# Kernel optimization log

Measured on AMD Instinct MI355X. Metric: run time of the kernel, lower is better.

Reference implementation:

```python
import jax, jax.numpy as jnp
import numpy as np

N_QUBITS = 8
DEPTH = 1
INPUT_DIM = 64
HIDDEN = 8  # must equal N_QUBITS
SEQ = 64
BATCH = 256


def _apply_rx(state, wire, ang):
    # state: (B, 2, 2, ..., 2) with wire w on axis 1+w; ang: (B,) angles
    n = state.ndim - 1
    st = jnp.moveaxis(state, 1 + wire, -1)
    a0, a1 = st[..., 0], st[..., 1]
    half = ang * 0.5
    c = jnp.cos(half).reshape((-1,) + (1,) * (n - 1))
    s = jnp.sin(half).reshape((-1,) + (1,) * (n - 1))
    new = jnp.stack([c * a0 - 1j * s * a1, c * a1 - 1j * s * a0], axis=-1)
    return jnp.moveaxis(new, -1, 1 + wire)


def _apply_cnot(state, cw, tw):
    st = jnp.moveaxis(state, (1 + cw, 1 + tw), (-2, -1))
    st = st.at[..., 1, :].set(st[..., 1, ::-1])  # flip target where control=1
    return jnp.moveaxis(st, (-2, -1), (1 + cw, 1 + tw))


def qgate(theta, qparams):
    # theta: (B, n) data-dependent RX angles; qparams: (n,) trainable RX angles
    B, n = theta.shape
    state = jnp.zeros((B,) + (2,) * n, dtype=jnp.complex64)
    state = state.at[(slice(None),) + (0,) * n].set(1.0 + 0.0j)  # |0...0>
    for w in range(n):
        state = _apply_rx(state, w, theta[:, w])
    for w in range(n - 1):
        state = _apply_cnot(state, w, w + 1)
    for w in range(n):
        state = _apply_rx(state, w, jnp.broadcast_to(qparams[w], (B,)))
    probs = jnp.abs(state) ** 2  # (B, 2, ..., 2)
    expz = []
    for w in range(n):
        pw = probs.sum(axis=tuple(a for a in range(1, n + 1) if a != 1 + w))  # (B, 2)
        expz.append(pw[:, 0] - pw[:, 1])  # <Z_w>
    return jnp.stack(expz, axis=1)  # (B, n)


def setup_inputs() -> dict:
    key = jax.random.key(0)
    ks = jax.random.split(key, 13)
    d_in = INPUT_DIM + HIDDEN
    d_out = N_QUBITS * DEPTH
    sc = 1.0 / np.sqrt(d_in)
    inp = {"inputs": jax.random.normal(ks[0], (SEQ, BATCH, INPUT_DIM), dtype=jnp.float32)}
    names = ["f", "i", "g", "o"]
    for j, nm in enumerate(names):
        inp["W" + nm] = jax.random.uniform(ks[1 + 3 * j], (d_out, d_in), minval=-sc, maxval=sc, dtype=jnp.float32)
        inp["b" + nm] = jax.random.uniform(ks[2 + 3 * j], (d_out,), minval=-sc, maxval=sc, dtype=jnp.float32)
        inp["q" + nm] = jax.random.normal(ks[3 + 3 * j], (d_out,), dtype=jnp.float32)
    return inp


def reference(inputs, Wf, bf, qf, Wi, bi, qi, Wg, bg, qg, Wo, bo, qo):
    B = inputs.shape[1]
    hx0 = jnp.zeros((B, HIDDEN), dtype=inputs.dtype)
    cx0 = jnp.zeros((B, HIDDEN), dtype=inputs.dtype)

    def step(carry, x_t):
        hx, cx = carry
        comb = jnp.concatenate([x_t, hx], axis=1)  # (B, input+hidden)
        f = jax.nn.sigmoid(qgate(comb @ Wf.T + bf, qf))
        i_ = jax.nn.sigmoid(qgate(comb @ Wi.T + bi, qi))
        g = jnp.tanh(qgate(comb @ Wg.T + bg, qg))
        o = jax.nn.sigmoid(qgate(comb @ Wo.T + bo, qo))
        cx = f * cx + i_ * g
        hx = o * jnp.tanh(cx)
        return (hx, cx), hx

    (hx, cx), outputs = jax.lax.scan(step, (hx0, cx0), inputs)
    return outputs, (hx, cx)
```

## Files before the change

### kernel.cpp

```cpp
#include <hip/hip_runtime.h>
#include <hip/hip_bf16.h>

__device__ float g_pre_static[8 * 1024 * 1024];

__device__ __forceinline__ float rcp_(float x)   { return __builtin_amdgcn_rcpf(x); }
__device__ __forceinline__ float sigm_f(float x) { return rcp_(1.0f + __expf(-x)); }
__device__ __forceinline__ float tanh_f(float x) { return 1.0f - 2.0f*rcp_(__expf(2.0f*x) + 1.0f); }
__device__ __forceinline__ float sigm(float x)  { return 1.0f/(1.0f + __expf(-x)); }
__device__ __forceinline__ float tanh_(float x) { float e = __expf(2.0f*x); return (e-1.0f)/(e+1.0f); }

template<int CTRL>
__device__ __forceinline__ float dppf(float x) {
    return __int_as_float(__builtin_amdgcn_update_dpp(
        0, __float_as_int(x), CTRL, 0xF, 0xF, true));
}

template<int IDD>
__global__ __launch_bounds__(512) void k_fused8(
    const float* __restrict__ x_,
    const float* __restrict__ W0, const float* __restrict__ b0p, const float* __restrict__ q0v,
    const float* __restrict__ W1, const float* __restrict__ b1p, const float* __restrict__ q1v,
    const float* __restrict__ W2, const float* __restrict__ b2p, const float* __restrict__ q2v,
    const float* __restrict__ W3, const float* __restrict__ b3p, const float* __restrict__ q3v,
    float* __restrict__ out, int S, int B)
{
    constexpr int DIN  = IDD + 8;
    constexpr int SMAX = 64;
    constexpr int TCH  = 32;
    __shared__ float xs[4][TCH][IDD];
    __shared__ float ps[SMAX][4][32];

    const int tid = threadIdx.x;
    const long b0 = (long)blockIdx.x * 4;
    const float* Wp[4] = {W0, W1, W2, W3};
    const float* bp[4] = {b0p, b1p, b2p, b3p};
    const float* qp[4] = {q0v, q1v, q2v, q3v};

    const int l  = tid & 31;
    const int b4 = (tid >> 5) & 3;
    const int hh = tid >> 7;
    const int gp = l >> 4, w8 = (l >> 1) & 7, e = l & 1;
    const int g  = 2*gp + e;

    float wr[IDD];
    {
        const float4* wv = (const float4*)(Wp[g] + (long)w8*DIN);
        #pragma unroll
        for (int k4 = 0; k4 < IDD/4; ++k4) {
            float4 v = wv[k4];
            wr[4*k4] = v.x; wr[4*k4+1] = v.y; wr[4*k4+2] = v.z; wr[4*k4+3] = v.w;
        }
    }
    const float bias = bp[g][w8];

    for (int c = 0; c < S; c += TCH) {
        {
            const int nf4 = 4 * TCH * (IDD/4);
            for (int idx = tid; idx < nf4; idx += 512) {
                int k4 = idx & (IDD/4 - 1);
                int r  = idx >> 4;
                int bs = r >> 5;
                int tl = r & (TCH - 1);
                int t  = c + tl; if (t >= S) t = S - 1;
                long bb = b0 + bs; if (bb >= B) bb = B - 1;
                float4 v = ((const float4*)(x_ + ((long)t*B + bb)*IDD))[k4];
                ((float4*)&xs[bs][tl][0])[k4] = v;
            }
        }
        __syncthreads();
        #pragma unroll
        for (int i = 0; i < TCH/4; ++i) {
            int t = c + hh*(TCH/4) + i;
            if (t < S) {
                const float4* xv = (const float4*)&xs[b4][t - c][0];
                float a0 = bias, a1 = 0.0f, a2 = 0.0f, a3 = 0.0f;
                #pragma unroll
                for (int k4 = 0; k4 < IDD/4; ++k4) {
                    float4 v = xv[k4];
                    a0 = fmaf(wr[4*k4],   v.x, a0);
                    a1 = fmaf(wr[4*k4+1], v.y, a1);
                    a2 = fmaf(wr[4*k4+2], v.z, a2);
                    a3 = fmaf(wr[4*k4+3], v.w, a3);
                }
                ps[t][b4][l] = (a0 + a1) + (a2 + a3);
            }
        }
        __syncthreads();
    }

    if (tid >= 64) return;

    const int lane = tid;
    const int w    = lane & 7;
    const int gpr  = (lane >> 3) & 1;
    const long b   = b0 + (lane >> 4);
    const int g0 = 2*gpr, g1 = 2*gpr + 1;

    float wrot0[8], wrot1[8];
    #pragma unroll
    for (int k = 0; k < 8; ++k) {
        int j = (w - k) & 7;
        wrot0[k] = Wp[g0][(long)w*DIN + IDD + j];
        wrot1[k] = Wp[g1][(long)w*DIN + IDD + j];
    }
    const float qv0 = qp[g0][w], qv1 = qp[g1][w];
    const float mult0 = (w < 7) ? __cosf(qv0) : 1.0f;
    const float mult1 = (w < 7) ? __cosf(qv1) : 1.0f;
    const float qadd0 = (w == 7) ? qv0 : 0.0f;
    const float qadd1 = (w == 7) ? qv1 : 0.0f;
    const float ascl = gpr ? 2.0f : 1.0f;
    const float aoff = gpr ? -1.0f : 0.0f;

    float cxw = 0.0f, hxw = 0.0f;
    float hxr[8];
    #pragma unroll
    for (int k = 0; k < 8; ++k) hxr[k] = 0.0f;

    const float2* pbase = (const float2*)(&ps[0][lane >> 4][gpr*16 + 2*w]);

    float2 pn = pbase[0];
    #pragma unroll 2
    for (int t = 0; t < S; ++t) {
        float2 pc = pn;
        int tn = (t + 1 < S) ? (t + 1) : (S - 1);
        pn = pbase[(long)tn * 64];

        float tA0 = pc.x, tA1 = pc.y, tB0, tB1;
        tA0 = fmaf(wrot0[0], hxr[0], tA0);  tA1 = fmaf(wrot1[0], hxr[0], tA1);
        tA0 = fmaf(wrot0[1], hxr[1], tA0);  tA1 = fmaf(wrot1[1], hxr[1], tA1);
        tA0 = fmaf(wrot0[2], hxr[2], tA0);  tA1 = fmaf(wrot1[2], hxr[2], tA1);
        tA0 = fmaf(wrot0[3], hxr[3], tA0);  tA1 = fmaf(wrot1[3], hxr[3], tA1);
        tB0 = wrot0[4]*hxr[4];              tB1 = wrot1[4]*hxr[4];
        tB0 = fmaf(wrot0[5], hxr[5], tB0);  tB1 = fmaf(wrot1[5], hxr[5], tB1);
        tB0 = fmaf(wrot0[6], hxr[6], tB0);  tB1 = fmaf(wrot1[6], hxr[6], tB1);
        tB0 = fmaf(wrot0[7], hxr[7], tB0);  tB1 = fmaf(wrot1[7], hxr[7], tB1);
        float th0 = tA0 + tB0;
        float th1 = tA1 + tB1;

        float P0 = __cosf(th0 + qadd0);
        float P1 = __cosf(th1 + qadd1);

        float s;
        s = dppf<0x111>(P0); P0 *= (w >= 1) ? s : 1.0f;
        s = dppf<0x111>(P1); P1 *= (w >= 1) ? s : 1.0f;
        s = dppf<0x112>(P0); P0 *= (w >= 2) ? s : 1.0f;
        s = dppf<0x112>(P1); P1 *= (w >= 2) ? s : 1.0f;
        s = dppf<0x114>(P0); P0 *= (w >= 4) ? s : 1.0f;
        s = dppf<0x114>(P1); P1 *= (w >= 4) ? s : 1.0f;

        float act0 = ascl * sigm_f(ascl * (mult0 * P0)) + aoff;
        float act1 = sigm_f(mult1 * P1);

        float ex0 = dppf<0x128>(act0);
        float ex1 = dppf<0x128>(act1);
        float fv = gpr ? ex0  : act0;
        float iv = gpr ? ex1  : act1;
        float gv = gpr ? act0 : ex0;
        float ov = gpr ? act1 : ex1;

        cxw = fv*cxw + iv*gv;
        hxw = ov * tanh_f(cxw);

        if (gpr == 0 && b < B) out[((long)t*B + b)*8 + w] = hxw;

        hxr[0] = hxw;
        hxr[1] = dppf<0x121>(hxw);
        hxr[2] = dppf<0x122>(hxw);
        hxr[3] = dppf<0x123>(hxw);
        hxr[4] = dppf<0x124>(hxw);
        hxr[5] = dppf<0x125>(hxw);
        hxr[6] = dppf<0x126>(hxw);
        hxr[7] = dppf<0x127>(hxw);
    }

    if (gpr == 0 && b < B) {
        out[((long)S*B + b)*8 + w]     = hxw;
        out[((long)S*B + B + b)*8 + w] = cxw;
    }
}

template<int IDD>
__global__ __launch_bounds__(256) void k_pre8(
    const float* __restrict__ x_,
    const float* __restrict__ W0, const float* __restrict__ b0p,
    const float* __restrict__ W1, const float* __restrict__ b1p,
    const float* __restrict__ W2, const float* __restrict__ b2p,
    const float* __restrict__ W3, const float* __restrict__ b3p,
    float* __restrict__ pre, int S, int B)
{
    constexpr int DIN = IDD + 8;
    __shared__ float xs[8][IDD];
    const int t   = blockIdx.x;
    const int tid = threadIdx.x;
    const int bl  = tid >> 5;
    const int l   = tid & 31;
    const int gp  = l >> 4, w = (l >> 1) & 7, e = l & 1;
    const int g   = 2*gp + e;
    const long b0 = (long)blockIdx.y * 8;
    const float* Wp[4] = {W0, W1, W2, W3};
    const float* bp[4] = {b0p, b1p, b2p, b3p};

    if (tid < 8*(IDD/4)) {
        int r = tid / (IDD/4), k4 = tid % (IDD/4);
        long bb = b0 + r; if (bb >= B) bb = B - 1;
        float4 v = ((const float4*)(x_ + ((long)t*B + bb)*IDD))[k4];
        ((float4*)&xs[r][0])[k4] = v;
    }

    float wr[IDD];
    {
        const float4* wv = (const float4*)(Wp[g] + (long)w*DIN);
        #pragma unroll
        for (int k4 = 0; k4 < IDD/4; ++k4) {
            float4 v = wv[k4];
            wr[4*k4] = v.x; wr[4*k4+1] = v.y; wr[4*k4+2] = v.z; wr[4*k4+3] = v.w;
        }
    }
    float a = bp[g][w];
    __syncthreads();

    const long b = b0 + bl;
    if (b >= B) return;
    const float4* xv = (const float4*)&xs[bl][0];
    #pragma unroll
    for (int k4 = 0; k4 < IDD/4; ++k4) {
        float4 v = xv[k4];
        a += wr[4*k4]*v.x + wr[4*k4+1]*v.y + wr[4*k4+2]*v.z + wr[4*k4+3]*v.w;
    }
    pre[((long)t*B + b)*32 + l] = a;
}

__global__ __launch_bounds__(256) void k_pre_gen(
    const float* __restrict__ x_,
    const float* W0, const float* b0p,
    const float* W1, const float* b1p,
    const float* W2, const float* b2p,
    const float* W3, const float* b3p,
    float* __restrict__ pre,
    int S, int B, int ID, int H, int SP)
{
    extern __shared__ float lds[];
    const int dIn  = ID + H;
    const int dInP = dIn + 1;
    float* xs    = lds;
    float* wsh   = lds + 64*SP;
    float* sbias = wsh + 4*H*dInP;
    const int t   = blockIdx.x;
    const int tid = threadIdx.x;
    const int bl  = tid & 63;
    const int q   = tid >> 6;
    const int b0  = blockIdx.y * 64;
    const float* Wp[4] = {W0, W1, W2, W3};
    const float* bp[4] = {b0p, b1p, b2p, b3p};

    for (int g = 0; g < 4; ++g)
        for (int idx = tid; idx < H*dIn; idx += 256) {
            int w = idx / dIn, k = idx - w*dIn;
            wsh[(g*H + w)*dInP + k] = Wp[g][idx];
        }
    for (int idx = tid; idx < 4*H; idx += 256)
        sbias[idx] = bp[idx / H][idx % H];

    {
        int total = 64 * ID;
        for (int i = tid; i < total; i += 256) {
            int r = i / ID, c = i - r*ID;
            long bb = (long)b0 + r; if (bb >= B) bb = B - 1;
            xs[r*SP + c] = x_[((long)t*B + bb)*ID + c];
        }
    }
    __syncthreads();

    const int b = b0 + bl;
    if (b < B) {
        const float* xrow = &xs[bl*SP];
        float* orow = pre + (((long)t*B + b)*4 + q)*H;
        for (int w = 0; w < H; ++w) {
            float acc = sbias[q*H + w];
            const float* wrow = &wsh[(q*H + w)*dInP];
            for (int k = 0; k < ID; ++k) acc += xrow[k] * wrow[k];
            orow[w] = acc;
        }
    }
}

__global__ __launch_bounds__(64) void k_rec8(
    const float* __restrict__ W0, const float* __restrict__ q0,
    const float* __restrict__ W1, const float* __restrict__ q1,
    const float* __restrict__ W2, const float* __restrict__ q2,
    const float* __restrict__ W3, const float* __restrict__ q3,
    const float* __restrict__ pre,
    float* __restrict__ out, int S, int B, int ID)
{
    const int dIn  = ID + 8;
    const int lane = threadIdx.x;
    const int w    = lane & 7;
    const int gp   = (lane >> 3) & 1;
    const int b    = blockIdx.x*4 + (lane >> 4);
    const int bs   = (b < B) ? b : (B - 1);
    const float* Wp[4] = {W0, W1, W2, W3};
    const float* qp[4] = {q0, q1, q2, q3};
    const int g0 = 2*gp, g1 = 2*gp + 1;

    float wrot0[8], wrot1[8];
    #pragma unroll
    for (int k = 0; k < 8; ++k) {
        int j = (w - k) & 7;
        wrot0[k] = Wp[g0][(long)w*dIn + ID + j];
        wrot1[k] = Wp[g1][(long)w*dIn + ID + j];
    }
    const float qv0 = qp[g0][w], qv1 = qp[g1][w];
    const float mult0 = (w < 7) ? __cosf(qv0) : 1.0f;
    const float mult1 = (w < 7) ? __cosf(qv1) : 1.0f;
    const float qadd0 = (w == 7) ? qv0 : 0.0f;
    const float qadd1 = (w == 7) ? qv1 : 0.0f;
    const float ascl = gp ? 2.0f : 1.0f;
    const float aoff = gp ? -1.0f : 0.0f;

    float cxw = 0.0f, hxw = 0.0f;
    float hxr[8];
    #pragma unroll
    for (int k = 0; k < 8; ++k) hxr[k] = 0.0f;

    const float2* base = (const float2*)(pre + (long)bs*32 + gp*16 + 2*w);
    const long tstep = (long)B*16;

    float2 pf[4];
    #pragma unroll
    for (int d = 0; d < 4; ++d) {
        int tt = (d < S) ? d : (S - 1);
        pf[d] = base[(long)tt*tstep];
    }

    for (int t0 = 0; t0 < S; t0 += 4) {
        #pragma unroll
        for (int d = 0; d < 4; ++d) {
            const int t = t0 + d;
            if (t < S) {
                float2 pc = pf[d];
                int tn = t + 4; if (tn >= S) tn = S - 1;
                pf[d] = base[(long)tn*tstep];

                float th0 = pc.x, th1 = pc.y;
                #pragma unroll
                for (int k = 0; k < 8; ++k) {
                    th0 = fmaf(wrot0[k], hxr[k], th0);
                    th1 = fmaf(wrot1[k], hxr[k], th1);
                }
                float P0 = __cosf(th0 + qadd0);
                float P1 = __cosf(th1 + qadd1);

                float s;
                s = dppf<0x111>(P0); P0 *= (w >= 1) ? s : 1.0f;
                s = dppf<0x111>(P1); P1 *= (w >= 1) ? s : 1.0f;
                s = dppf<0x112>(P0); P0 *= (w >= 2) ? s : 1.0f;
                s = dppf<0x112>(P1); P1 *= (w >= 2) ? s : 1.0f;
                s = dppf<0x114>(P0); P0 *= (w >= 4) ? s : 1.0f;
                s = dppf<0x114>(P1); P1 *= (w >= 4) ? s : 1.0f;

                float act0 = ascl * sigm_f(ascl * (mult0 * P0)) + aoff;
                float act1 = sigm_f(mult1 * P1);

                float ex0 = dppf<0x128>(act0);
                float ex1 = dppf<0x128>(act1);
                float fv = gp ? ex0  : act0;
                float iv = gp ? ex1  : act1;
                float gv = gp ? act0 : ex0;
                float ov = gp ? act1 : ex1;

                cxw = fv*cxw + iv*gv;
                hxw = ov * tanh_f(cxw);

                if (gp == 0 && b < B) out[((long)t*B + b)*8 + w] = hxw;

                hxr[0] = hxw;
                hxr[1] = dppf<0x121>(hxw);
                hxr[2] = dppf<0x122>(hxw);
                hxr[3] = dppf<0x123>(hxw);
                hxr[4] = dppf<0x124>(hxw);
                hxr[5] = dppf<0x125>(hxw);
                hxr[6] = dppf<0x126>(hxw);
                hxr[7] = dppf<0x127>(hxw);
            }
        }
    }

    if (gp == 0 && b < B) {
        out[((long)S*B + b)*8 + w]     = hxw;
        out[((long)S*B + B + b)*8 + w] = cxw;
    }
}

__global__ __launch_bounds__(64) void k_rec_g(
    const float* __restrict__ pre,
    const float* W0, const float* q0,
    const float* W1, const float* q1,
    const float* W2, const float* q2,
    const float* W3, const float* q3,
    float* __restrict__ out, int S, int B, int ID, int H)
{
    __shared__ float sWh[4*32*32];
    __shared__ float scq[4*32];
    const int dIn = ID + H;
    const int tid = threadIdx.x;
    const int b   = blockIdx.x*64 + tid;
    const float* Wp[4] = {W0, W1, W2, W3};
    const float* qp[4] = {q0, q1, q2, q3};

    for (int idx = tid; idx < 4*H*H; idx += 64) {
        int g = idx / (H*H), r = idx % (H*H);
        int w = r / H, j = r % H;
        sWh[(g*H + w)*H + j] = Wp[g][(long)w*dIn + ID + j];
    }
    for (int idx = tid; idx < 4*H; idx += 64) {
        int g = idx / H, w = idx % H;
        float qv = qp[g][w];
        scq[idx] = (w < H-1) ? __cosf(qv) : qv;
    }
    __syncthreads();
    if (b >= B) return;

    float hx[32], cx[32], gate[4][32], th[32];
    for (int w = 0; w < H; ++w) { hx[w] = 0.0f; cx[w] = 0.0f; }

    for (int t = 0; t < S; ++t) {
        const float* pt = pre + ((long)t*B + b)*4*H;
        for (int g = 0; g < 4; ++g) {
            for (int w = 0; w < H; ++w) {
                float a = pt[g*H + w];
                const float* wrp = &sWh[(g*H + w)*H];
                for (int j = 0; j < H; ++j) a += wrp[j]*hx[j];
                th[w] = a;
            }
            float cum = 1.0f;
            for (int w = 0; w < H-1; ++w) {
                cum *= __cosf(th[w]);
                gate[g][w] = scq[g*H + w] * cum;
            }
            gate[g][H-1] = cum * __cosf(th[H-1] + scq[g*H + H-1]);
        }
        float* orow = out + ((long)t*B + b)*H;
        for (int w = 0; w < H; ++w) {
            float fv = sigm (gate[0][w]);
            float iv = sigm (gate[1][w]);
            float gv = tanh_(gate[2][w]);
            float ov = sigm (gate[3][w]);
            cx[w] = fv*cx[w] + iv*gv;
            hx[w] = ov*tanh_(cx[w]);
            orow[w] = hx[w];
        }
    }
    float* oh = out + ((long)S*B + b)*H;
    float* oc = out + ((long)S*B + B + b)*H;
    for (int w = 0; w < H; ++w) { oh[w] = hx[w]; oc[w] = cx[w]; }
}

static bool derive(long sz[13], long osz, long& S, long& B, long& ID, long& H) {
    H = sz[3];
    long dIn = (H > 0) ? sz[1] / H : 0;
    ID = dIn - H;
    long TB = (ID > 0) ? sz[0] / ID : 0;
    B = (H > 0) ? (osz / H - TB) / 2 : 0;
    S = (B > 0) ? TB / B : 0;
    return (H >= 1 && H <= 32 && ID >= 1 && B >= 1 && S >= 1 &&
            S*B == TB && (S*B + 2*B)*H == osz &&
            dIn*H == sz[1] && TB*ID == sz[0]);
}

extern "C" void kernel_launch(void* const* d_in, const int* in_sizes, int n_in,
                              void* d_out, int out_size, void* d_ws, size_t ws_size,
                              hipStream_t stream) {
    const float* x  = (const float*)d_in[0];
    const float* Wf = (const float*)d_in[1];  const float* bfv = (const float*)d_in[2];  const float* qf = (const float*)d_in[3];
    const float* Wi = (const float*)d_in[4];  const float* biv = (const float*)d_in[5];  const float* qi = (const float*)d_in[6];
    const float* Wg = (const float*)d_in[7];  const float* bgv = (const float*)d_in[8];  const float* qg = (const float*)d_in[9];
    const float* Wo = (const float*)d_in[10]; const float* bov = (const float*)d_in[11]; const float* qo = (const float*)d_in[12];
    float* out = (float*)d_out;

    long S = 0, B = 0, ID = 0, H = 0;
    bool ok = false;
    for (int scale : {1, 4, 2}) {
        long sz[13];
        for (int i = 0; i < 13; ++i) sz[i] = (long)in_sizes[i] / scale;
        long osz = (long)out_size / scale;
        if (derive(sz, osz, S, B, ID, H)) { ok = true; break; }
    }
    if (!ok) { H = 8; ID = 64; B = 256; S = 64; }
    long dIn = ID + H;

    if (H == 8 && ID == 64 && S <= 64) {
        k_fused8<64><<<dim3((unsigned)((B + 3) / 4)), dim3(512), 0, stream>>>(
            x, Wf, bfv, qf, Wi, biv, qi, Wg, bgv, qg, Wo, bov, qo,
            out, (int)S, (int)B);
        return;
    }

    size_t pre_bytes = (size_t)S * 4 * H * B * sizeof(float);
    float* pre = (ws_size >= pre_bytes) ? (float*)d_ws : g_pre_static;

    if (H == 8 && ID == 64) {
        k_pre8<64><<<dim3((unsigned)S, (unsigned)((B + 7) / 8)), dim3(256), 0, stream>>>(
            x, Wf, bfv, Wi, biv, Wg, bgv, Wo, bov, pre, (int)S, (int)B);
        k_rec8<<<dim3((unsigned)((B + 3) / 4)), dim3(64), 0, stream>>>(
            Wf, qf, Wi, qi, Wg, qg, Wo, qo, pre, out, (int)S, (int)B, (int)ID);
    } else {
        int SP = (int)ID + 1;
        size_t lds_bytes = (size_t)(64*SP + 4*H*(dIn + 1) + 4*H) * sizeof(float);
        k_pre_gen<<<dim3((unsigned)S, (unsigned)((B + 63) / 64)), dim3(256), lds_bytes, stream>>>(
            x, Wf, bfv, Wi, biv, Wg, bgv, Wo, bov, pre,
            (int)S, (int)B, (int)ID, (int)H, SP);
        k_rec_g<<<dim3((unsigned)((B + 63) / 64)), dim3(64), 0, stream>>>(
            pre, Wf, qf, Wi, qi, Wg, qg, Wo, qo, out, (int)S, (int)B, (int)ID, (int)H);
    }
}
```

Baseline: 102.8 us.

## Overlap recurrence with input projection using a dedicated recurrence wavefront

Adds a ninth wavefront (576 threads) that runs the serial LSTM recurrence for the previous time chunk while the other 512 threads compute the input projection for the current chunk. The chunk size is halved to 16 so the pipeline has more stages. The goal is to hide the projection phase behind the sequential recurrence instead of running the two back to back. In exchange there is an extra barrier per chunk, and the recurrence is now split into chunks with loop-carried state, which may add overhead.

```diff
diff --git a/kernel.cpp b/kernel.cpp
--- a/kernel.cpp
+++ b/kernel.cpp
@@ -16,7 +16,7 @@
 }
 
 template<int IDD>
-__global__ __launch_bounds__(512) void k_fused8(
+__global__ __launch_bounds__(576) void k_fused8(
     const float* __restrict__ x_,
     const float* __restrict__ W0, const float* __restrict__ b0p, const float* __restrict__ q0v,
     const float* __restrict__ W1, const float* __restrict__ b1p, const float* __restrict__ q1v,
@@ -26,7 +26,7 @@
 {
     constexpr int DIN  = IDD + 8;
     constexpr int SMAX = 64;
-    constexpr int TCH  = 32;
+    constexpr int TCH  = 16;
     __shared__ float xs[4][TCH][IDD];
     __shared__ float ps[SMAX][4][32];
 
@@ -36,146 +36,161 @@
     const float* bp[4] = {b0p, b1p, b2p, b3p};
     const float* qp[4] = {q0v, q1v, q2v, q3v};
 
-    const int l  = tid & 31;
-    const int b4 = (tid >> 5) & 3;
-    const int hh = tid >> 7;
-    const int gp = l >> 4, w8 = (l >> 1) & 7, e = l & 1;
-    const int g  = 2*gp + e;
+    const int l   = tid & 31;
+    const int b4g = (tid >> 5) & 3;
+    const int sub = (tid >> 7) & 3;
+    const int gp  = l >> 4, w8 = (l >> 1) & 7, e = l & 1;
+    const int g   = 2*gp + e;
 
     float wr[IDD];
-    {
+    float bias = 0.0f;
+    if (tid < 512) {
         const float4* wv = (const float4*)(Wp[g] + (long)w8*DIN);
         #pragma unroll
         for (int k4 = 0; k4 < IDD/4; ++k4) {
             float4 v = wv[k4];
             wr[4*k4] = v.x; wr[4*k4+1] = v.y; wr[4*k4+2] = v.z; wr[4*k4+3] = v.w;
         }
-    }
-    const float bias = bp[g][w8];
-
-    for (int c = 0; c < S; c += TCH) {
+        bias = bp[g][w8];
+    }
+
+    const int lane = tid & 63;
+    const int w    = lane & 7;
+    const int gpr  = (lane >> 3) & 1;
+    const long bb_ = b0 + (lane >> 4);
+    const int g0 = 2*gpr, g1 = 2*gpr + 1;
+
+    float wrot0[8], wrot1[8];
+    float mult0 = 1.0f, mult1 = 1.0f, qadd0 = 0.0f, qadd1 = 0.0f;
+    if (tid >= 512) {
+        #pragma unroll
+        for (int k = 0; k < 8; ++k) {
+            int j = (w - k) & 7;
+            wrot0[k] = Wp[g0][(long)w*DIN + IDD + j];
+            wrot1[k] = Wp[g1][(long)w*DIN + IDD + j];
+        }
+        float qv0 = qp[g0][w], qv1 = qp[g1][w];
+        mult0 = (w < 7) ? __cosf(qv0) : 1.0f;
+        mult1 = (w < 7) ? __cosf(qv1) : 1.0f;
+        qadd0 = (w == 7) ? qv0 : 0.0f;
+        qadd1 = (w == 7) ? qv1 : 0.0f;
+    }
+    const float ascl = gpr ? 2.0f : 1.0f;
+    const float aoff = gpr ? -1.0f : 0.0f;
+
+    float cxw = 0.0f, hxw = 0.0f;
+    float hxr[8];
+    #pragma unroll
+    for (int k = 0; k < 8; ++k) hxr[k] = 0.0f;
+
+    const float2* pbase = (const float2*)(&ps[0][lane >> 4][gpr*16 + 2*w]);
+
+    auto rec_run = [&](int t0e, int t1e) {
+        float2 pn = pbase[(long)t0e * 64];
+        for (int t = t0e; t < t1e; ++t) {
+            float2 pc = pn;
+            int tn = (t + 1 < t1e) ? (t + 1) : t;
+            pn = pbase[(long)tn * 64];
+
+            float tA0 = pc.x, tA1 = pc.y, tB0, tB1;
+            tA0 = fmaf(wrot0[0], hxr[0], tA0);  tA1 = fmaf(wrot1[0], hxr[0], tA1);
+            tA0 = fmaf(wrot0[1], hxr[1], tA0);  tA1 = fmaf(wrot1[1], hxr[1], tA1);
+            tA0 = fmaf(wrot0[2], hxr[2], tA0);  tA1 = fmaf(wrot1[2], hxr[2], tA1);
+            tA0 = fmaf(wrot0[3], hxr[3], tA0);  tA1 = fmaf(wrot1[3], hxr[3], tA1);
+            tB0 = wrot0[4]*hxr[4];              tB1 = wrot1[4]*hxr[4];
+            tB0 = fmaf(wrot0[5], hxr[5], tB0);  tB1 = fmaf(wrot1[5], hxr[5], tB1);
+            tB0 = fmaf(wrot0[6], hxr[6], tB0);  tB1 = fmaf(wrot1[6], hxr[6], tB1);
+            tB0 = fmaf(wrot0[7], hxr[7], tB0);  tB1 = fmaf(wrot1[7], hxr[7], tB1);
+            float th0 = tA0 + tB0;
+            float th1 = tA1 + tB1;
+
+            float P0 = __cosf(th0 + qadd0);
+            float P1 = __cosf(th1 + qadd1);
+
+            float s;
+            s = dppf<0x111>(P0); P0 *= (w >= 1) ? s : 1.0f;
+            s = dppf<0x111>(P1); P1 *= (w >= 1) ? s : 1.0f;
+            s = dppf<0x112>(P0); P0 *= (w >= 2) ? s : 1.0f;
+            s = dppf<0x112>(P1); P1 *= (w >= 2) ? s : 1.0f;
+            s = dppf<0x114>(P0); P0 *= (w >= 4) ? s : 1.0f;
+            s = dppf<0x114>(P1); P1 *= (w >= 4) ? s : 1.0f;
+
+            float act0 = ascl * sigm_f(ascl * (mult0 * P0)) + aoff;
+            float act1 = sigm_f(mult1 * P1);
+
+            float ex0 = dppf<0x128>(act0);
+            float ex1 = dppf<0x128>(act1);
+            float fv = gpr ? ex0  : act0;
+            float iv = gpr ? ex1  : act1;
+            float gv = gpr ? act0 : ex0;
+            float ov = gpr ? act1 : ex1;
+
+            cxw = fv*cxw + iv*gv;
+            hxw = ov * tanh_f(cxw);
+
+            if (gpr == 0 && bb_ < B) out[((long)t*B + bb_)*8 + w] = hxw;
+
+            hxr[0] = hxw;
+            hxr[1] = dppf<0x121>(hxw);
+            hxr[2] = dppf<0x122>(hxw);
+            hxr[3] = dppf<0x123>(hxw);
+            hxr[4] = dppf<0x124>(hxw);
+            hxr[5] = dppf<0x125>(hxw);
+            hxr[6] = dppf<0x126>(hxw);
+            hxr[7] = dppf<0x127>(hxw);
+        }
+    };
+
+    const int nch = (S + TCH - 1) / TCH;
+    for (int c = 0; c < nch; ++c) {
         {
             const int nf4 = 4 * TCH * (IDD/4);
-            for (int idx = tid; idx < nf4; idx += 512) {
-                int k4 = idx & (IDD/4 - 1);
-                int r  = idx >> 4;
-                int bs = r >> 5;
-                int tl = r & (TCH - 1);
-                int t  = c + tl; if (t >= S) t = S - 1;
+            for (int idx = tid; idx < nf4; idx += 576) {
+                int k4 = idx % (IDD/4);
+                int r  = idx / (IDD/4);
+                int bs = r / TCH;
+                int tl = r % TCH;
+                int t  = c*TCH + tl; if (t >= S) t = S - 1;
                 long bb = b0 + bs; if (bb >= B) bb = B - 1;
                 float4 v = ((const float4*)(x_ + ((long)t*B + bb)*IDD))[k4];
                 ((float4*)&xs[bs][tl][0])[k4] = v;
             }
         }
         __syncthreads();
-        #pragma unroll
-        for (int i = 0; i < TCH/4; ++i) {
-            int t = c + hh*(TCH/4) + i;
-            if (t < S) {
-                const float4* xv = (const float4*)&xs[b4][t - c][0];
-                float a0 = bias, a1 = 0.0f, a2 = 0.0f, a3 = 0.0f;
-                #pragma unroll
-                for (int k4 = 0; k4 < IDD/4; ++k4) {
-                    float4 v = xv[k4];
-                    a0 = fmaf(wr[4*k4],   v.x, a0);
-                    a1 = fmaf(wr[4*k4+1], v.y, a1);
-                    a2 = fmaf(wr[4*k4+2], v.z, a2);
-                    a3 = fmaf(wr[4*k4+3], v.w, a3);
+
+        if (tid < 512) {
+            #pragma unroll
+            for (int i = 0; i < TCH/4; ++i) {
+                int t = c*TCH + sub*(TCH/4) + i;
+                if (t < S) {
+                    const float4* xv = (const float4*)&xs[b4g][t - c*TCH][0];
+                    float a0 = bias, a1 = 0.0f, a2 = 0.0f, a3 = 0.0f;
+                    #pragma unroll
+                    for (int k4 = 0; k4 < IDD/4; ++k4) {
+                        float4 v = xv[k4];
+                        a0 = fmaf(wr[4*k4],   v.x, a0);
+                        a1 = fmaf(wr[4*k4+1], v.y, a1);
+                        a2 = fmaf(wr[4*k4+2], v.z, a2);
+                        a3 = fmaf(wr[4*k4+3], v.w, a3);
+                    }
+                    ps[t][b4g][l] = (a0 + a1) + (a2 + a3);
                 }
-                ps[t][b4][l] = (a0 + a1) + (a2 + a3);
             }
+        } else if (c > 0) {
+            int t0e = (c - 1) * TCH;
+            int t1e = c * TCH; if (t1e > S) t1e = S;
+            rec_run(t0e, t1e);
         }
         __syncthreads();
     }
 
-    if (tid >= 64) return;
-
-    const int lane = tid;
-    const int w    = lane & 7;
-    const int gpr  = (lane >> 3) & 1;
-    const long b   = b0 + (lane >> 4);
-    const int g0 = 2*gpr, g1 = 2*gpr + 1;
-
-    float wrot0[8], wrot1[8];
-    #pragma unroll
-    for (int k = 0; k < 8; ++k) {
-        int j = (w - k) & 7;
-        wrot0[k] = Wp[g0][(long)w*DIN + IDD + j];
-        wrot1[k] = Wp[g1][(long)w*DIN + IDD + j];
-    }
-    const float qv0 = qp[g0][w], qv1 = qp[g1][w];
-    const float mult0 = (w < 7) ? __cosf(qv0) : 1.0f;
-    const float mult1 = (w < 7) ? __cosf(qv1) : 1.0f;
-    const float qadd0 = (w == 7) ? qv0 : 0.0f;
-    const float qadd1 = (w == 7) ? qv1 : 0.0f;
-    const float ascl = gpr ? 2.0f : 1.0f;
-    const float aoff = gpr ? -1.0f : 0.0f;
-
-    float cxw = 0.0f, hxw = 0.0f;
-    float hxr[8];
-    #pragma unroll
-    for (int k = 0; k < 8; ++k) hxr[k] = 0.0f;
-
-    const float2* pbase = (const float2*)(&ps[0][lane >> 4][gpr*16 + 2*w]);
-
-    float2 pn = pbase[0];
-    #pragma unroll 2
-    for (int t = 0; t < S; ++t) {
-        float2 pc = pn;
-        int tn = (t + 1 < S) ? (t + 1) : (S - 1);
-        pn = pbase[(long)tn * 64];
-
-        float tA0 = pc.x, tA1 = pc.y, tB0, tB1;
-        tA0 = fmaf(wrot0[0], hxr[0], tA0);  tA1 = fmaf(wrot1[0], hxr[0], tA1);
-        tA0 = fmaf(wrot0[1], hxr[1], tA0);  tA1 = fmaf(wrot1[1], hxr[1], tA1);
-        tA0 = fmaf(wrot0[2], hxr[2], tA0);  tA1 = fmaf(wrot1[2], hxr[2], tA1);
-        tA0 = fmaf(wrot0[3], hxr[3], tA0);  tA1 = fmaf(wrot1[3], hxr[3], tA1);
-        tB0 = wrot0[4]*hxr[4];              tB1 = wrot1[4]*hxr[4];
-        tB0 = fmaf(wrot0[5], hxr[5], tB0);  tB1 = fmaf(wrot1[5], hxr[5], tB1);
-        tB0 = fmaf(wrot0[6], hxr[6], tB0);  tB1 = fmaf(wrot1[6], hxr[6], tB1);
-        tB0 = fmaf(wrot0[7], hxr[7], tB0);  tB1 = fmaf(wrot1[7], hxr[7], tB1);
-        float th0 = tA0 + tB0;
-        float th1 = tA1 + tB1;
-
-        float P0 = __cosf(th0 + qadd0);
-        float P1 = __cosf(th1 + qadd1);
-
-        float s;
-        s = dppf<0x111>(P0); P0 *= (w >= 1) ? s : 1.0f;
-        s = dppf<0x111>(P1); P1 *= (w >= 1) ? s : 1.0f;
-        s = dppf<0x112>(P0); P0 *= (w >= 2) ? s : 1.0f;
-        s = dppf<0x112>(P1); P1 *= (w >= 2) ? s : 1.0f;
-        s = dppf<0x114>(P0); P0 *= (w >= 4) ? s : 1.0f;
-        s = dppf<0x114>(P1); P1 *= (w >= 4) ? s : 1.0f;
-
-        float act0 = ascl * sigm_f(ascl * (mult0 * P0)) + aoff;
-        float act1 = sigm_f(mult1 * P1);
-
-        float ex0 = dppf<0x128>(act0);
-        float ex1 = dppf<0x128>(act1);
-        float fv = gpr ? ex0  : act0;
-        float iv = gpr ? ex1  : act1;
-        float gv = gpr ? act0 : ex0;
-        float ov = gpr ? act1 : ex1;
-
-        cxw = fv*cxw + iv*gv;
-        hxw = ov * tanh_f(cxw);
-
-        if (gpr == 0 && b < B) out[((long)t*B + b)*8 + w] = hxw;
-
-        hxr[0] = hxw;
-        hxr[1] = dppf<0x121>(hxw);
-        hxr[2] = dppf<0x122>(hxw);
-        hxr[3] = dppf<0x123>(hxw);
-        hxr[4] = dppf<0x124>(hxw);
-        hxr[5] = dppf<0x125>(hxw);
-        hxr[6] = dppf<0x126>(hxw);
-        hxr[7] = dppf<0x127>(hxw);
-    }
-
-    if (gpr == 0 && b < B) {
-        out[((long)S*B + b)*8 + w]     = hxw;
-        out[((long)S*B + B + b)*8 + w] = cxw;
+    if (tid >= 512) {
+        int t0e = (nch - 1) * TCH;
+        if (t0e < S) rec_run(t0e, S);
+        if (gpr == 0 && bb_ < B) {
+            out[((long)S*B + bb_)*8 + w]     = hxw;
+            out[((long)S*B + B + bb_)*8 + w] = cxw;
+        }
     }
 }
 
@@ -489,7 +504,7 @@
     long dIn = ID + H;
 
     if (H == 8 && ID == 64 && S <= 64) {
-        k_fused8<64><<<dim3((unsigned)((B + 3) / 4)), dim3(512), 0, stream>>>(
+        k_fused8<64><<<dim3((unsigned)((B + 3) / 4)), dim3(576), 0, stream>>>(
             x, Wf, bfv, qf, Wi, biv, qi, Wg, bgv, qg, Wo, bov, qo,
             out, (int)S, (int)B);
         return;
```

After: 100.3 us. 2.4% less time.
